# Kernel optimization log

Measured on AMD Instinct MI355X. Metric: run time of the kernel, lower is better.

Reference implementation:

```python
import jax, jax.numpy as jnp
import numpy as np

DIM = 256
N = 16          # number of sub-codebooks
K = 1024        # codes per sub-codebook (torch arg K; SeqVQ uses self.embedding directly)
E_DIM = DIM // N
DEPTH = 3
BETA = 0.25
B = 8192


def setup_inputs() -> dict:
    key = jax.random.key(0)
    k1, k2, k3 = jax.random.split(key, 3)
    z = jax.random.normal(k1, (B, DIM), dtype=jnp.float32)
    # nn.init.uniform_(data, -1/N, 1/N)
    embedding = jax.random.uniform(k2, (N, K, E_DIM), dtype=jnp.float32,
                                   minval=-1.0 / N, maxval=1.0 / N)
    # frozen-twin pooling query encoder: mean over depth then Linear D->D
    W = jax.random.normal(k3, (DIM, DIM), dtype=jnp.float32) * 0.02
    b = jnp.zeros((DIM,), dtype=jnp.float32)
    return {"z": z, "embedding": embedding, "W": W, "b": b}


def reference(z, embedding, W, b):
    Bq, D = z.shape
    n, k, e = embedding.shape
    zr = z.reshape(Bq, n, e)                 # residual, squeezed (B,N,1,e)->(B,N,e)
    e_sq = jnp.sum(embedding * embedding, axis=-1)  # (N,K)
    z_q_steps = []
    onehot = None
    idx = None
    for _ in range(DEPTH):
        # cdist((B,N,1,e),(N,K,e)) via ||z||^2 - 2 z.e + ||e||^2, then sqrt
        z_sq = jnp.sum(zr * zr, axis=-1)                       # (B,N)
        cross = jnp.einsum('bne,nke->bnk', zr, embedding)      # (B,N,K)
        d = jnp.sqrt(jnp.maximum(z_sq[:, :, None] - 2.0 * cross + e_sq[None], 0.0))
        idx = jnp.argmin(d, axis=-1)                           # (B,N)
        onehot = jax.nn.one_hot(idx, k, dtype=z.dtype)         # scatter one-hot (B,N,K)
        q = jnp.einsum('bnk,nke->bne', onehot, embedding)      # (B,N,e)
        zr = zr - q
        z_q_steps.append(q.reshape(Bq, D))
    z_q_residual = jnp.stack(z_q_steps, axis=1)                # (B, depth, D)
    # frozen twin query encoder (params carry no gradient in original)
    Wc = jax.lax.stop_gradient(W)
    bc = jax.lax.stop_gradient(b)
    z_q = jnp.mean(z_q_residual, axis=1) @ Wc + bc             # (B, D)
    loss = (jnp.mean((jax.lax.stop_gradient(z_q) - z) ** 2)
            + BETA * jnp.mean((z_q - jax.lax.stop_gradient(z)) ** 2))
    z_q_out = z + jax.lax.stop_gradient(z_q - z)               # straight-through
    return loss, z_q_out, onehot, idx[:, :, None]
```

## Files before the change

kernel.cpp:

```cpp
#include <hip/hip_runtime.h>
#include <math.h>

#define BQ    8192
#define DIMD  256
#define NSUB  16
#define KC    1024
#define ED    16
#define SCW   32

#define OFF_ZQ   1
#define OFF_OH   (1 + BQ * DIMD)
#define OH_ELEMS (BQ * NSUB * KC)
#define OFF_IDX  (OFF_OH + OH_ELEMS)
#define F4N      ((OH_ELEMS - 4) / 4)
#define NTHR     (1024 * 256)

typedef __attribute__((ext_vector_type(2))) float v2f;
typedef __attribute__((ext_vector_type(4))) float f32x4;
typedef __attribute__((ext_vector_type(8))) short bshort8;
typedef __attribute__((ext_vector_type(4))) unsigned int u32x4;

struct Zr  { v2f p0, p1, p2, p3, p4, p5, p6, p7; };
struct Row { float4 c0, c1, c2, c3; };
struct V2x2 { v2f lo, hi; };

__device__ __forceinline__ float np_sumsq(Zr z) {
  float q0 = __fmul_rn(z.p0.x, z.p0.x), q1 = __fmul_rn(z.p0.y, z.p0.y);
  float q2 = __fmul_rn(z.p1.x, z.p1.x), q3 = __fmul_rn(z.p1.y, z.p1.y);
  float q4 = __fmul_rn(z.p2.x, z.p2.x), q5 = __fmul_rn(z.p2.y, z.p2.y);
  float q6 = __fmul_rn(z.p3.x, z.p3.x), q7 = __fmul_rn(z.p3.y, z.p3.y);
  float q8 = __fmul_rn(z.p4.x, z.p4.x), q9 = __fmul_rn(z.p4.y, z.p4.y);
  float qa = __fmul_rn(z.p5.x, z.p5.x), qb = __fmul_rn(z.p5.y, z.p5.y);
  float qc = __fmul_rn(z.p6.x, z.p6.x), qd = __fmul_rn(z.p6.y, z.p6.y);
  float qe = __fmul_rn(z.p7.x, z.p7.x), qf = __fmul_rn(z.p7.y, z.p7.y);
  float r0 = __fadd_rn(q0, q8), r1 = __fadd_rn(q1, q9);
  float r2 = __fadd_rn(q2, qa), r3 = __fadd_rn(q3, qb);
  float r4 = __fadd_rn(q4, qc), r5 = __fadd_rn(q5, qd);
  float r6 = __fadd_rn(q6, qe), r7 = __fadd_rn(q7, qf);
  return __fadd_rn(__fadd_rn(__fadd_rn(r0, r1), __fadd_rn(r2, r3)),
                   __fadd_rn(__fadd_rn(r4, r5), __fadd_rn(r6, r7)));
}

__device__ __forceinline__ float ref_d(Zr z, Row rw, float zsq, float esq) {
  float p0  = __fmul_rn(z.p0.x, rw.c0.x), p1  = __fmul_rn(z.p0.y, rw.c0.y);
  float p2  = __fmul_rn(z.p1.x, rw.c0.z), p3  = __fmul_rn(z.p1.y, rw.c0.w);
  float p4  = __fmul_rn(z.p2.x, rw.c1.x), p5  = __fmul_rn(z.p2.y, rw.c1.y);
  float p6  = __fmul_rn(z.p3.x, rw.c1.z), p7  = __fmul_rn(z.p3.y, rw.c1.w);
  float p8  = __fmul_rn(z.p4.x, rw.c2.x), p9  = __fmul_rn(z.p4.y, rw.c2.y);
  float p10 = __fmul_rn(z.p5.x, rw.c2.z), p11 = __fmul_rn(z.p5.y, rw.c2.w);
  float p12 = __fmul_rn(z.p6.x, rw.c3.x), p13 = __fmul_rn(z.p6.y, rw.c3.y);
  float p14 = __fmul_rn(z.p7.x, rw.c3.z), p15 = __fmul_rn(z.p7.y, rw.c3.w);
  float L0 = __fadd_rn(__fadd_rn(__fadd_rn(p0, p4), p8),  p12);
  float L1 = __fadd_rn(__fadd_rn(__fadd_rn(p1, p5), p9),  p13);
  float L2 = __fadd_rn(__fadd_rn(__fadd_rn(p2, p6), p10), p14);
  float L3 = __fadd_rn(__fadd_rn(__fadd_rn(p3, p7), p11), p15);
  float cross = __fadd_rn(__fadd_rn(L0, L1), __fadd_rn(L2, L3));
  float t = __fsub_rn(zsq, __fmul_rn(2.0f, cross));
  t = __fadd_rn(t, esq);
  t = fmaxf(t, 0.0f);
  return (float)sqrt((double)t);
}

__device__ __forceinline__ float fastv_s(Zr z, Row rw, float eh) {
  V2x2 a0 = __builtin_bit_cast(V2x2, rw.c0);
  V2x2 a1 = __builtin_bit_cast(V2x2, rw.c1);
  V2x2 a2 = __builtin_bit_cast(V2x2, rw.c2);
  V2x2 a3 = __builtin_bit_cast(V2x2, rw.c3);
  v2f accA = {eh, 0.f}, accB = {0.f, 0.f};
  accA = __builtin_elementwise_fma(-z.p0, a0.lo, accA);
  accB = __builtin_elementwise_fma(-z.p1, a0.hi, accB);
  accA = __builtin_elementwise_fma(-z.p2, a1.lo, accA);
  accB = __builtin_elementwise_fma(-z.p3, a1.hi, accB);
  accA = __builtin_elementwise_fma(-z.p4, a2.lo, accA);
  accB = __builtin_elementwise_fma(-z.p5, a2.hi, accB);
  accA = __builtin_elementwise_fma(-z.p6, a3.lo, accA);
  accB = __builtin_elementwise_fma(-z.p7, a3.hi, accB);
  v2f acc = accA + accB;
  return acc.x + acc.y;
}

__device__ __forceinline__ Zr sub_row(Zr z, Row rw) {
  Zr o;
  o.p0 = (v2f){__fsub_rn(z.p0.x, rw.c0.x), __fsub_rn(z.p0.y, rw.c0.y)};
  o.p1 = (v2f){__fsub_rn(z.p1.x, rw.c0.z), __fsub_rn(z.p1.y, rw.c0.w)};
  o.p2 = (v2f){__fsub_rn(z.p2.x, rw.c1.x), __fsub_rn(z.p2.y, rw.c1.y)};
  o.p3 = (v2f){__fsub_rn(z.p3.x, rw.c1.z), __fsub_rn(z.p3.y, rw.c1.w)};
  o.p4 = (v2f){__fsub_rn(z.p4.x, rw.c2.x), __fsub_rn(z.p4.y, rw.c2.y)};
  o.p5 = (v2f){__fsub_rn(z.p5.x, rw.c2.z), __fsub_rn(z.p5.y, rw.c2.w)};
  o.p6 = (v2f){__fsub_rn(z.p6.x, rw.c3.x), __fsub_rn(z.p6.y, rw.c3.y)};
  o.p7 = (v2f){__fsub_rn(z.p7.x, rw.c3.z), __fsub_rn(z.p7.y, rw.c3.w)};
  return o;
}

__device__ __forceinline__ Zr load_zr(const float* p) {
  const float4* zp = (const float4*)p;
  float4 a0 = zp[0], a1 = zp[1], a2 = zp[2], a3 = zp[3];
  V2x2 v0 = __builtin_bit_cast(V2x2, a0), v1 = __builtin_bit_cast(V2x2, a1);
  V2x2 v2 = __builtin_bit_cast(V2x2, a2), v3 = __builtin_bit_cast(V2x2, a3);
  Zr z;
  z.p0 = v0.lo; z.p1 = v0.hi; z.p2 = v1.lo; z.p3 = v1.hi;
  z.p4 = v2.lo; z.p5 = v2.hi; z.p6 = v3.lo; z.p7 = v3.hi;
  return z;
}

__device__ __forceinline__ Row load_row(const float* p) {
  const float4* cp = (const float4*)p;
  Row rw; rw.c0 = cp[0]; rw.c1 = cp[1]; rw.c2 = cp[2]; rw.c3 = cp[3];
  return rw;
}

__device__ __forceinline__ float l1norm(Zr z) {
  float t0 = fabsf(z.p0.x) + fabsf(z.p0.y), t1 = fabsf(z.p1.x) + fabsf(z.p1.y);
  float t2 = fabsf(z.p2.x) + fabsf(z.p2.y), t3 = fabsf(z.p3.x) + fabsf(z.p3.y);
  float t4 = fabsf(z.p4.x) + fabsf(z.p4.y), t5 = fabsf(z.p5.x) + fabsf(z.p5.y);
  float t6 = fabsf(z.p6.x) + fabsf(z.p6.y), t7 = fabsf(z.p7.x) + fabsf(z.p7.y);
  return ((t0 + t1) + (t2 + t3)) + ((t4 + t5) + (t6 + t7));
}

__device__ __forceinline__ unsigned int f2bf(float x) {
  unsigned int u = __float_as_uint(x);
  return (u + 0x7FFFu + ((u >> 16) & 1u)) >> 16;
}
__device__ __forceinline__ float bf2f(unsigned int b) {
  return __uint_as_float(b << 16);
}

__device__ __forceinline__ void stage_zr(Zr zr, unsigned int* zqp, float* zbp) {
  v2f* zb2 = (v2f*)zbp;
  zb2[0]=zr.p0; zb2[1]=zr.p1; zb2[2]=zr.p2; zb2[3]=zr.p3;
  zb2[4]=zr.p4; zb2[5]=zr.p5; zb2[6]=zr.p6; zb2[7]=zr.p7;
  v2f P; unsigned h0, h1, l0, l1;
#define PK(I, PP)                                                             \
  P = PP; h0 = f2bf(P.x); h1 = f2bf(P.y); zqp[I] = h0 | (h1 << 16);           \
  l0 = f2bf(__fsub_rn(P.x, bf2f(h0))); l1 = f2bf(__fsub_rn(P.y, bf2f(h1)));   \
  zqp[8 + I] = l0 | (l1 << 16);
  PK(0, zr.p0) PK(1, zr.p1) PK(2, zr.p2) PK(3, zr.p3)
  PK(4, zr.p4) PK(5, zr.p5) PK(6, zr.p6) PK(7, zr.p7)
#undef PK
}

__global__ void vq_prep(const float* __restrict__ emb,
                        unsigned int* __restrict__ ws) {
  const int row = blockIdx.x * 256 + threadIdx.x;
  const float* c = emb + row * 16;
  unsigned int o[16];
#pragma unroll
  for (int u = 0; u < 8; ++u) {
    float a = -c[2 * u], b = -c[2 * u + 1];
    unsigned int h0 = f2bf(a), h1 = f2bf(b);
    o[u] = h0 | (h1 << 16);
    unsigned int l0 = f2bf(__fsub_rn(a, bf2f(h0)));
    unsigned int l1 = f2bf(__fsub_rn(b, bf2f(h1)));
    o[8 + u] = l0 | (l1 << 16);
  }
  u32x4* dst = (u32x4*)ws + row * 4;
#pragma unroll
  for (int j = 0; j < 4; ++j)
    dst[j] = (u32x4){o[4 * j], o[4 * j + 1], o[4 * j + 2], o[4 * j + 3]};
  float* esqg = (float*)(ws + 16384 * 16);
  esqg[row] = np_sumsq(load_zr(c));
}

__global__ __launch_bounds__(256, 4) void vq_main(
    const float* __restrict__ z, const float* __restrict__ emb,
    const unsigned int* __restrict__ ws, float* __restrict__ out) {
  __shared__ float esq[KC];
  __shared__ float ehs[KC];
  __shared__ unsigned int zq[4 * SCW * 16];
  __shared__ float zb[4 * SCW * 16];
  const int tid   = threadIdx.x;
  const int bx    = blockIdx.x;
  const int n     = bx & 15;
  const int bbase = (bx >> 4) * 128;
  const int w     = tid >> 6;
  const int lane  = tid & 63;
  const int q     = lane >> 4;
  const int c16   = lane & 15;
  const int sc    = lane & 31;
  const float* embn = emb + n * (KC * ED);
  const u32x4* wsn  = (const u32x4*)ws + n * (KC * 4);
  const float* esqg = (const float*)(ws + 16384 * 16) + n * KC;

  for (int k = tid; k < KC; k += 256) {
    float s = esqg[k];
    esq[k] = s; ehs[k] = 0.5f * s;
  }
  if (bx == 0 && tid == 0) {
    out[0] = 0.f;
    out[OFF_OH + 0] = 0.f; out[OFF_OH + 1] = 0.f; out[OFF_OH + 2] = 0.f;
    out[OFF_OH + OH_ELEMS - 1] = 0.f;
  }
  __syncthreads();

  const int scanB = bbase + w * SCW + sc;
  Zr zr = load_zr(z + scanB * DIMD + n * ED);
  unsigned int* zqw = zq + w * (SCW * 16);
  float*        zbw = zb + w * (SCW * 16);
  if (lane < SCW) stage_zr(zr, zqw + sc * 16, zbw + sc * 16);

  const int gtid = bx * 256 + tid;
  f32x4* f4 = (f32x4*)(out + OFF_OH + 3);
  const f32x4 zf4 = {0.f, 0.f, 0.f, 0.f};
  int sIdx = 0, fcnt = 0;
  int bi = 0;

  for (int dep = 0; dep < 3; ++dep) {
    asm volatile("s_waitcnt lgkmcnt(0)" ::: "memory");
    u32x4 B0u = *(const u32x4*)(zqw + ((0 * 16 + c16) * 16 + q * 4));
    u32x4 B1u = *(const u32x4*)(zqw + ((1 * 16 + c16) * 16 + q * 4));
    bshort8 b0 = __builtin_bit_cast(bshort8, B0u);
    bshort8 b1 = __builtin_bit_cast(bshort8, B1u);

    float m1_0 = 3.0e38f, m1_1 = 3.0e38f;
    float m2_0 = 3.0e38f, m2_1 = 3.0e38f;
    int   k1_0 = 0, k1_1 = 0;
    const int qc4 = q * 4;
    const int aoff = c16 * 4 + q, boff = c16 * 4 + ((q + 2) & 3);

    u32x4 A1n = wsn[aoff], A2n = wsn[boff];
    float4 ehn = ((const float4*)ehs)[q];

    for (int ct = 0; ct < 64; ++ct) {
      u32x4 A1c = A1n, A2c = A2n;
      f32x4 ehv = __builtin_bit_cast(f32x4, ehn);
      if (ct < 63) {
        const int nb = (ct + 1) * 64;
        A1n = wsn[nb + aoff];
        A2n = wsn[nb + boff];
        ehn = ((const float4*)ehs)[(ct + 1) * 4 + q];
      }
      if (fcnt != 2) {
        int sl = sIdx * NTHR + gtid; ++sIdx;
        if (sl < F4N) __builtin_nontemporal_store(zf4, f4 + sl);
      }
      fcnt = (fcnt == 2) ? 0 : fcnt + 1;
      bshort8 a1 = __builtin_bit_cast(bshort8, A1c);
      bshort8 a2 = __builtin_bit_cast(bshort8, A2c);
      const int cbase = ct * 16 + qc4;
#define UPD(V, CODE, M1, K1, M2)                                              \
      { float v_ = (V);                                                       \
        M2 = __builtin_amdgcn_fmed3f(v_, M1, M2);                             \
        bool lt_ = v_ < M1; M1 = lt_ ? v_ : M1; K1 = lt_ ? (CODE) : K1; }
#define DOST(BV, M1, K1, M2)                                                  \
      { f32x4 d1 = __builtin_amdgcn_mfma_f32_16x16x32_bf16(a1, BV, ehv, 0,0,0);\
        f32x4 dd = __builtin_amdgcn_mfma_f32_16x16x32_bf16(a2, BV, d1, 0,0,0);\
        UPD(dd.x, cbase + 0, M1, K1, M2)                                      \
        UPD(dd.y, cbase + 1, M1, K1, M2)                                      \
        UPD(dd.z, cbase + 2, M1, K1, M2)                                      \
        UPD(dd.w, cbase + 3, M1, K1, M2) }
      DOST(b0, m1_0, k1_0, m2_0)
      DOST(b1, m1_1, k1_1, m2_1)
#undef DOST
#undef UPD
    }
#define MERGE3(M1, K1, M2, OFF)                                               \
    { float om = __shfl_xor(M1, OFF); int ok = __shfl_xor(K1, OFF);           \
      float os = __shfl_xor(M2, OFF);                                         \
      float hi = fmaxf(M1, om);                                               \
      M2 = fminf(fminf(M2, os), hi);                                          \
      bool bw = (om < M1) || (om == M1 && ok < K1);                           \
      M1 = bw ? om : M1; K1 = bw ? ok : K1; }
    MERGE3(m1_0, k1_0, m2_0, 16) MERGE3(m1_0, k1_0, m2_0, 32)
    MERGE3(m1_1, k1_1, m2_1, 16) MERGE3(m1_1, k1_1, m2_1, 32)
#undef MERGE3
    const bool t1 = (sc >= 16);
    float m1F = t1 ? m1_1 : m1_0;
    float m2F = t1 ? m2_1 : m2_0;
    int   k1F = t1 ? k1_1 : k1_0;

    const float wepsb = fmaf(l1norm(zr), 1.0e-6f, 1.5e-5f);
    bool fb = (lane < SCW) && (__fsub_rn(m2F, m1F) < wepsb);
    unsigned long long mask = __ballot(fb);
    while (mask) {
      int ss = __ffsll((unsigned long long)mask) - 1;
      mask &= (mask - 1);
      Zr zs = load_zr(zbw + ss * 16);
      float zsq = np_sumsq(zs);
      float gme = __shfl(m1F, ss) + __shfl(wepsb, ss);
      float db = 3.0e38f; int kb = 0;
      for (int i = 0; i < 16; ++i) {
        int kk = i * 64 + lane;
        Row rw = load_row(embn + kk * 16);
        if (fastv_s(zs, rw, ehs[kk]) < gme) {
          float d = ref_d(zs, rw, zsq, esq[kk]);
          if (d < db) { db = d; kb = kk; }
        }
      }
#pragma unroll
      for (int off = 1; off < 64; off <<= 1) {
        float od = __shfl_xor(db, off); int ok = __shfl_xor(kb, off);
        if (od < db || (od == db && ok < kb)) { db = od; kb = ok; }
      }
      if (lane == ss) k1F = kb;
    }
    k1F = __shfl(k1F, sc);
    bi = k1F;
    zr = sub_row(zr, load_row(embn + k1F * 16));
    if (dep < 2 && lane < SCW) stage_zr(zr, zqw + sc * 16, zbw + sc * 16);
  }
  for (; sIdx < 128; ++sIdx) {
    int sl = sIdx * NTHR + gtid;
    if (sl < F4N) __builtin_nontemporal_store(zf4, f4 + sl);
  }
  if (lane < SCW) {
    out[OFF_IDX + scanB * NSUB + n] = (float)bi;
    Zr zo = load_zr(z + scanB * DIMD + n * ED);
    float* mp2 = out + OFF_ZQ + scanB * DIMD + n * ED;
    mp2[0]  = __fdiv_rn(__fsub_rn(zo.p0.x, zr.p0.x), 3.0f);
    mp2[1]  = __fdiv_rn(__fsub_rn(zo.p0.y, zr.p0.y), 3.0f);
    mp2[2]  = __fdiv_rn(__fsub_rn(zo.p1.x, zr.p1.x), 3.0f);
    mp2[3]  = __fdiv_rn(__fsub_rn(zo.p1.y, zr.p1.y), 3.0f);
    mp2[4]  = __fdiv_rn(__fsub_rn(zo.p2.x, zr.p2.x), 3.0f);
    mp2[5]  = __fdiv_rn(__fsub_rn(zo.p2.y, zr.p2.y), 3.0f);
    mp2[6]  = __fdiv_rn(__fsub_rn(zo.p3.x, zr.p3.x), 3.0f);
    mp2[7]  = __fdiv_rn(__fsub_rn(zo.p3.y, zr.p3.y), 3.0f);
    mp2[8]  = __fdiv_rn(__fsub_rn(zo.p4.x, zr.p4.x), 3.0f);
    mp2[9]  = __fdiv_rn(__fsub_rn(zo.p4.y, zr.p4.y), 3.0f);
    mp2[10] = __fdiv_rn(__fsub_rn(zo.p5.x, zr.p5.x), 3.0f);
    mp2[11] = __fdiv_rn(__fsub_rn(zo.p5.y, zr.p5.y), 3.0f);
    mp2[12] = __fdiv_rn(__fsub_rn(zo.p6.x, zr.p6.x), 3.0f);
    mp2[13] = __fdiv_rn(__fsub_rn(zo.p6.y, zr.p6.y), 3.0f);
    mp2[14] = __fdiv_rn(__fsub_rn(zo.p7.x, zr.p7.x), 3.0f);
    mp2[15] = __fdiv_rn(__fsub_rn(zo.p7.y, zr.p7.y), 3.0f);
  }
}

__global__ void vq_ones(float* __restrict__ out) {
  int g = blockIdx.x * 256 + threadIdx.x;
  int k = (int)out[OFF_IDX + g];
  out[OFF_OH + g * KC + k] = 1.0f;
}

#define TB 16
__global__ __launch_bounds__(256, 2) void vq_head(
    const float* __restrict__ z, const float* __restrict__ W,
    const float* __restrict__ bias, float* __restrict__ out) {
  __shared__ float ml[TB][DIMD];
  __shared__ double reds[4];
  const int t  = threadIdx.x;
  const int r0 = blockIdx.x * TB;
  for (int j = t; j < TB * DIMD; j += 256) {
    int r = j >> 8, d = j & 255;
    ml[r][d] = out[OFF_ZQ + (r0 + r) * DIMD + d];
  }
  __syncthreads();
  float acc[TB];
#pragma unroll
  for (int r = 0; r < TB; ++r) acc[r] = 0.f;
  for (int d = 0; d < DIMD; ++d) {
    float w = W[d * DIMD + t];
#pragma unroll
    for (int r = 0; r < TB; ++r) acc[r] = fmaf(ml[r][d], w, acc[r]);
  }
  const float bv = bias[t];
  double lp = 0.0;
#pragma unroll
  for (int r = 0; r < TB; ++r) {
    float zq   = acc[r] + bv;
    float zv   = z[(r0 + r) * DIMD + t];
    float diff = zq - zv;
    out[OFF_ZQ + (r0 + r) * DIMD + t] = zv + diff;
    lp += (double)diff * (double)diff;
  }
#pragma unroll
  for (int o = 32; o > 0; o >>= 1) lp += __shfl_down(lp, o);
  if ((t & 63) == 0) reds[t >> 6] = lp;
  __syncthreads();
  if (t == 0) {
    double tot = reds[0] + reds[1] + reds[2] + reds[3];
    atomicAdd(out, (float)(tot * (1.25 / (double)(BQ * DIMD))));
  }
}

extern "C" void kernel_launch(void* const* d_in, const int* in_sizes, int n_in,
                              void* d_out, int out_size, void* d_ws, size_t ws_size,
                              hipStream_t stream) {
  const float* z    = (const float*)d_in[0];
  const float* emb  = (const float*)d_in[1];
  const float* W    = (const float*)d_in[2];
  const float* bias = (const float*)d_in[3];
  float* out = (float*)d_out;
  unsigned int* wsp = (unsigned int*)d_ws;
  vq_prep<<<dim3(64), dim3(256), 0, stream>>>(emb, wsp);
  vq_main<<<dim3((BQ / 128) * NSUB), dim3(256), 0, stream>>>(z, emb, wsp, out);
  vq_ones<<<dim3((BQ * NSUB) / 256), dim3(256), 0, stream>>>(out);
  vq_head<<<dim3(BQ / TB), dim3(256), 0, stream>>>(z, W, bias, out);
}
```

Baseline: 679.3 us.

## Split one-hot zero-fill into dedicated blocks and deepen codebook prefetch

Grid doubles: odd blocks only zero-fill the 512MB one-hot region with nontemporal stores, and even blocks run the VQ search without fill stores interleaved into the MFMA loop. The codebook tile prefetch also goes from one iteration ahead to two. This separates a bandwidth-bound stream from compute so both can run concurrently on different waves, at the cost of extra registers and different block scheduling.

```diff
diff --git a/kernel.cpp b/kernel.cpp
--- a/kernel.cpp
+++ b/kernel.cpp
@@ -13,7 +13,7 @@
 #define OH_ELEMS (BQ * NSUB * KC)
 #define OFF_IDX  (OFF_OH + OH_ELEMS)
 #define F4N      ((OH_ELEMS - 4) / 4)
-#define NTHR     (1024 * 256)
+#define FTHR     (1024 * 256)
 
 typedef __attribute__((ext_vector_type(2))) float v2f;
 typedef __attribute__((ext_vector_type(4))) float f32x4;
@@ -168,10 +168,24 @@
   __shared__ float ehs[KC];
   __shared__ unsigned int zq[4 * SCW * 16];
   __shared__ float zb[4 * SCW * 16];
-  const int tid   = threadIdx.x;
-  const int bx    = blockIdx.x;
-  const int n     = bx & 15;
-  const int bbase = (bx >> 4) * 128;
+  const int tid = threadIdx.x;
+  const int bx  = blockIdx.x;
+
+  if (bx & 1) {
+    const int fgtid = (bx >> 1) * 256 + tid;
+    f32x4* f4 = (f32x4*)(out + OFF_OH + 3);
+    const f32x4 zf4 = {0.f, 0.f, 0.f, 0.f};
+#pragma unroll 8
+    for (int s = 0; s < 128; ++s) {
+      int sl = s * FTHR + fgtid;
+      if (sl < F4N) __builtin_nontemporal_store(zf4, f4 + sl);
+    }
+    return;
+  }
+
+  const int cbx   = bx >> 1;
+  const int n     = cbx & 15;
+  const int bbase = (cbx >> 4) * 128;
   const int w     = tid >> 6;
   const int lane  = tid & 63;
   const int q     = lane >> 4;
@@ -185,7 +199,7 @@
     float s = esqg[k];
     esq[k] = s; ehs[k] = 0.5f * s;
   }
-  if (bx == 0 && tid == 0) {
+  if (cbx == 0 && tid == 0) {
     out[0] = 0.f;
     out[OFF_OH + 0] = 0.f; out[OFF_OH + 1] = 0.f; out[OFF_OH + 2] = 0.f;
     out[OFF_OH + OH_ELEMS - 1] = 0.f;
@@ -198,10 +212,6 @@
   float*        zbw = zb + w * (SCW * 16);
   if (lane < SCW) stage_zr(zr, zqw + sc * 16, zbw + sc * 16);
 
-  const int gtid = bx * 256 + tid;
-  f32x4* f4 = (f32x4*)(out + OFF_OH + 3);
-  const f32x4 zf4 = {0.f, 0.f, 0.f, 0.f};
-  int sIdx = 0, fcnt = 0;
   int bi = 0;
 
   for (int dep = 0; dep < 3; ++dep) {
@@ -217,23 +227,21 @@
     const int qc4 = q * 4;
     const int aoff = c16 * 4 + q, boff = c16 * 4 + ((q + 2) & 3);
 
-    u32x4 A1n = wsn[aoff], A2n = wsn[boff];
-    float4 ehn = ((const float4*)ehs)[q];
+    u32x4 A1p0 = wsn[aoff],      A2p0 = wsn[boff];
+    u32x4 A1p1 = wsn[64 + aoff], A2p1 = wsn[64 + boff];
+    float4 ehp0 = ((const float4*)ehs)[q];
+    float4 ehp1 = ((const float4*)ehs)[4 + q];
 
     for (int ct = 0; ct < 64; ++ct) {
-      u32x4 A1c = A1n, A2c = A2n;
-      f32x4 ehv = __builtin_bit_cast(f32x4, ehn);
-      if (ct < 63) {
-        const int nb = (ct + 1) * 64;
-        A1n = wsn[nb + aoff];
-        A2n = wsn[nb + boff];
-        ehn = ((const float4*)ehs)[(ct + 1) * 4 + q];
+      u32x4 A1c = A1p0, A2c = A2p0;
+      f32x4 ehv = __builtin_bit_cast(f32x4, ehp0);
+      A1p0 = A1p1; A2p0 = A2p1; ehp0 = ehp1;
+      if (ct < 62) {
+        const int nb = (ct + 2) * 64;
+        A1p1 = wsn[nb + aoff];
+        A2p1 = wsn[nb + boff];
+        ehp1 = ((const float4*)ehs)[(ct + 2) * 4 + q];
       }
-      if (fcnt != 2) {
-        int sl = sIdx * NTHR + gtid; ++sIdx;
-        if (sl < F4N) __builtin_nontemporal_store(zf4, f4 + sl);
-      }
-      fcnt = (fcnt == 2) ? 0 : fcnt + 1;
       bshort8 a1 = __builtin_bit_cast(bshort8, A1c);
       bshort8 a2 = __builtin_bit_cast(bshort8, A2c);
       const int cbase = ct * 16 + qc4;
@@ -298,10 +306,6 @@
     zr = sub_row(zr, load_row(embn + k1F * 16));
     if (dep < 2 && lane < SCW) stage_zr(zr, zqw + sc * 16, zbw + sc * 16);
   }
-  for (; sIdx < 128; ++sIdx) {
-    int sl = sIdx * NTHR + gtid;
-    if (sl < F4N) __builtin_nontemporal_store(zf4, f4 + sl);
-  }
   if (lane < SCW) {
     out[OFF_IDX + scanB * NSUB + n] = (float)bi;
     Zr zo = load_zr(z + scanB * DIMD + n * ED);
@@ -382,7 +386,7 @@
   float* out = (float*)d_out;
   unsigned int* wsp = (unsigned int*)d_ws;
   vq_prep<<<dim3(64), dim3(256), 0, stream>>>(emb, wsp);
-  vq_main<<<dim3((BQ / 128) * NSUB), dim3(256), 0, stream>>>(z, emb, wsp, out);
+  vq_main<<<dim3(2048), dim3(256), 0, stream>>>(z, emb, wsp, out);
   vq_ones<<<dim3((BQ * NSUB) / 256), dim3(256), 0, stream>>>(out);
   vq_head<<<dim3(BQ / TB), dim3(256), 0, stream>>>(z, W, bias, out);
 }
```

Result: slower. 748.0 us (+10.1%).
